# Performance work log

Hardware: AMD Instinct MI355X
Metric: run time of the kernel (lower is better)

Reference implementation:

```python
import jax, jax.numpy as jnp
import numpy as np

N_FQK, N_FV, N_REL, N_VAL, N_KNOW = 512, 256, 128, 64, 256
TOPK_QK, TOPK_V, TOPK_REL, TOPK_VAL = 64, 32, 16, 3
FQK_END = N_FQK
FV_END = N_FQK + N_FV
REL_END = FV_END + N_REL
VAL_END = REL_END + N_VAL
TOTAL = VAL_END + N_KNOW


def setup_inputs() -> dict:
    key = jax.random.key(0)
    k1, k2, k3, k4, k5 = jax.random.split(key, 5)
    B, S, D, DS = 8, 4096, 1024, 64
    x = jax.random.normal(k1, (B, S, D), dtype=jnp.float32)
    importance = jax.random.uniform(k2, (B, S), dtype=jnp.float32)
    proj_w = jax.random.normal(k3, (DS, D), dtype=jnp.float32) * (1.0 / np.sqrt(D))
    proj_b = jax.random.normal(k4, (DS,), dtype=jnp.float32) * 0.01
    neuron_emb = jax.random.normal(k5, (TOTAL, DS), dtype=jnp.float32) * 0.02
    return {"x": x, "importance": importance, "proj_w": proj_w,
            "proj_b": proj_b, "neuron_emb": neuron_emb}


def _topk_sparsify(w, k):
    # keep top-k values per row, zero elsewhere
    vals, idx = jax.lax.top_k(w, k)
    B = w.shape[0]
    sparse = jnp.zeros_like(w).at[jnp.arange(B)[:, None], idx].set(vals)
    return sparse, idx


def reference(x, importance, proj_w, proj_b, neuron_emb):
    # shared projection + normalized neuron embeddings (eval: dropout off,
    # no excitability bonus)
    h = jnp.einsum('bsd,kd->bsk', x, proj_w) + proj_b          # [B,S,d_space]
    emb_n = neuron_emb / jnp.linalg.norm(neuron_emb, axis=-1, keepdims=True)
    all_logits = jnp.einsum('bsk,nk->bsn', h, emb_n)            # [B,S,TOTAL]

    def agg(logits):
        pref = jax.nn.softmax(logits, axis=-1)                  # [B,S,n]
        return jnp.einsum('bs,bsn->bn', importance, pref)

    w_qk = agg(all_logits[..., :FQK_END])
    _, idx_qk = jax.lax.top_k(w_qk, TOPK_QK)
    idx_qk = jnp.sort(idx_qk, axis=-1)

    w_v = agg(all_logits[..., FQK_END:FV_END])
    _, idx_v = jax.lax.top_k(w_v, TOPK_V)
    idx_v = jnp.sort(idx_v, axis=-1)

    rel_logits = all_logits[..., FV_END:REL_END]
    # relational_Q and relational_K use the same logits slice (eval mode)
    rel_dense_Q = agg(rel_logits)
    rel_dense_K = agg(rel_logits)
    rel_Q, _ = _topk_sparsify(rel_dense_Q, TOPK_REL)
    rel_K, _ = _topk_sparsify(rel_dense_K, TOPK_REL)

    val_dense = agg(all_logits[..., REL_END:VAL_END])
    val_w, _ = _topk_sparsify(val_dense, TOPK_VAL)

    return idx_qk, idx_v, rel_Q, rel_K, val_w
```

## Files before the change

kernel.cpp:

```cpp
#include <hip/hip_runtime.h>


typedef short short8 __attribute__((ext_vector_type(8)));
typedef float f32x4 __attribute__((ext_vector_type(4)));
typedef unsigned int uint4v __attribute__((ext_vector_type(4)));

__device__ __forceinline__ unsigned short f32_to_bf16(float f) {
  unsigned u = __float_as_uint(f);
  u += 0x7FFF + ((u >> 16) & 1);
  return (unsigned short)(u >> 16);
}
__device__ __forceinline__ float bf16_to_f32(unsigned short h) {
  return __uint_as_float(((unsigned)h) << 16);
}

__device__ __forceinline__ unsigned cvt_pk_bf16(float a, float b) {
  unsigned r;
  asm("v_cvt_pk_bf16_f32 %0, %1, %2" : "=v"(r) : "v"(a), "v"(b));
  return r;
}

__device__ __forceinline__ void split8v(const f32x4& v0, const f32x4& v1,
                                        short8& hi, short8& lo) {
  unsigned hp[4], lp[4];
#pragma unroll
  for (int j = 0; j < 4; ++j) {
    float a = (j < 2) ? v0[2 * j] : v1[2 * j - 4];
    float b = (j < 2) ? v0[2 * j + 1] : v1[2 * j - 3];
    unsigned p = cvt_pk_bf16(a, b);
    float ra = a - __uint_as_float(p << 16);
    float rb = b - __uint_as_float(p & 0xFFFF0000u);
    hp[j] = p;
    lp[j] = cvt_pk_bf16(ra, rb);
  }
  hi = __builtin_bit_cast(short8, (uint4v){hp[0], hp[1], hp[2], hp[3]});
  lo = __builtin_bit_cast(short8, (uint4v){lp[0], lp[1], lp[2], lp[3]});
}

#define MFMA(a, b, c) __builtin_amdgcn_mfma_f32_16x16x32_bf16(a, b, c, 0, 0, 0)

typedef const __attribute__((address_space(1))) unsigned int guint;
typedef __attribute__((address_space(3))) unsigned int luint;
__device__ __forceinline__ void stage16(const float* g, float* l) {
  __builtin_amdgcn_global_load_lds((guint*)g, (luint*)l, 16, 0, 0);
}
__device__ __forceinline__ void bar() {
  asm volatile("" ::: "memory");
  __builtin_amdgcn_s_barrier();
  asm volatile("" ::: "memory");
}

__global__ __launch_bounds__(256) void k_prep(const float* __restrict__ pw,
                                              const float* __restrict__ emb,
                                              unsigned short* __restrict__ whi,
                                              unsigned short* __restrict__ wlo,
                                              unsigned short* __restrict__ ehi,
                                              unsigned short* __restrict__ elo,
                                              float* __restrict__ wg) {
  int tid = blockIdx.x * 256 + threadIdx.x;
  if (tid < 7680) wg[tid] = 0.f;
  for (int i = tid; i < 65536; i += gridDim.x * 256) {
    float v = pw[i];
    unsigned short h = f32_to_bf16(v);
    whi[i] = h;
    wlo[i] = f32_to_bf16(v - bf16_to_f32(h));
  }
  int wid = tid >> 6, lane = tid & 63;
  int nw = gridDim.x * 4;
  for (int n = wid; n < 960; n += nw) {
    float v = emb[n * 64 + lane];
    float s = v * v;
#pragma unroll
    for (int off = 1; off < 64; off <<= 1) s += __shfl_xor(s, off);
    float vn = v / sqrtf(s);
    unsigned short h = f32_to_bf16(vn);
    ehi[n * 64 + lane] = h;
    elo[n * 64 + lane] = f32_to_bf16(vn - bf16_to_f32(h));
  }
}

__global__ __launch_bounds__(256, 4) void k_main(
    const float* __restrict__ x, const unsigned short* __restrict__ whi,
    const unsigned short* __restrict__ wlo, const float* __restrict__ pb,
    const unsigned short* __restrict__ ehi, const unsigned short* __restrict__ elo,
    const float* __restrict__ imp, float* __restrict__ wg) {
  __shared__ __align__(16) float xt[5][32][32];
  __shared__ __align__(16) unsigned short hxh[32][64];
  __shared__ __align__(16) unsigned short hxl[32][64];
  __shared__ float zpart[4][32][4];
  __shared__ float coefL[32][4];

  const int tid = threadIdx.x, w = tid >> 6, lane = tid & 63;
  const int q = lane >> 4, c = lane & 15;
  const int row0 = blockIdx.x * 32;
  const int nt0 = w;

  const int srow = tid >> 3;
  const int scol = ((tid & 7) ^ (srow & 7)) * 4;
  const float* sbase = x + (size_t)(row0 + srow) * 1024 + scol;
  auto STAGEX = [&](int slot, int ks) {
    stage16(sbase + ks * 32, &xt[slot][0][0] + (w << 8));
  };

  const unsigned short* bwh = whi + (size_t)(nt0 * 16 + c) * 1024 + q * 8;
  const unsigned short* bwl = wlo + (size_t)(nt0 * 16 + c) * 1024 + q * 8;

  f32x4 acc0 = {0.f, 0.f, 0.f, 0.f}, acc1 = {0.f, 0.f, 0.f, 0.f};

  const unsigned sw = (unsigned)((c & 7) << 4);
  const unsigned off1 = ((unsigned)(q * 32)) ^ sw;
  const unsigned off2 = ((unsigned)(q * 32 + 16)) ^ sw;
  const char* xby = (const char*)&xt[0][0][0] + (size_t)c * 128;

  auto projstep = [&](int slot, short8 B_hi, short8 B_lo) {
    const char* bp = xby + slot * 4096;
    f32x4 a0 = *(const f32x4*)(bp + off1);
    f32x4 a1 = *(const f32x4*)(bp + off2);
    f32x4 a2 = *(const f32x4*)(bp + 2048 + off1);
    f32x4 a3 = *(const f32x4*)(bp + 2048 + off2);
    short8 ah, al;
    split8v(a0, a1, ah, al);
    acc0 = MFMA(ah, B_hi, acc0);
    acc0 = MFMA(ah, B_lo, acc0);
    acc0 = MFMA(al, B_hi, acc0);
    split8v(a2, a3, ah, al);
    acc1 = MFMA(ah, B_hi, acc1);
    acc1 = MFMA(ah, B_lo, acc1);
    acc1 = MFMA(al, B_hi, acc1);
  };

  short8 BhA[4], BlA[4], BhB[4], BlB[4];
#pragma unroll
  for (int kk = 0; kk < 4; ++kk) {
    BhA[kk] = *(const short8*)(bwh + kk * 32);
    BlA[kk] = *(const short8*)(bwl + kk * 32);
  }
  STAGEX(0, 0); STAGEX(1, 1); STAGEX(2, 2); STAGEX(3, 3);
  int rs = 0, wsl = 4;

  auto group = [&](int g, short8 (&ch)[4], short8 (&cl)[4],
                   short8 (&nh)[4], short8 (&nl)[4]) {
#pragma unroll
    for (int kk = 0; kk < 4; ++kk) {
      nh[kk] = *(const short8*)(bwh + ((g + 1) * 4 + kk) * 32);
      nl[kk] = *(const short8*)(bwl + ((g + 1) * 4 + kk) * 32);
    }
#pragma unroll
    for (int p = 0; p < 4; ++p) {
      asm volatile("s_waitcnt vmcnt(11)" ::: "memory");
      bar();
      STAGEX(wsl, 4 * g + p + 4);
      projstep(rs, ch[p], cl[p]);
      ++rs; if (rs == 5) rs = 0;
      ++wsl; if (wsl == 5) wsl = 0;
    }
  };
  group(0, BhA, BlA, BhB, BlB);
  group(1, BhB, BlB, BhA, BlA);
  group(2, BhA, BlA, BhB, BlB);
  group(3, BhB, BlB, BhA, BlA);
  group(4, BhA, BlA, BhB, BlB);
  group(5, BhB, BlB, BhA, BlA);
  group(6, BhA, BlA, BhB, BlB);
  asm volatile("s_waitcnt vmcnt(3)" ::: "memory"); bar();
  projstep(rs, BhB[0], BlB[0]); ++rs; if (rs == 5) rs = 0;
  asm volatile("s_waitcnt vmcnt(2)" ::: "memory"); bar();
  projstep(rs, BhB[1], BlB[1]); ++rs; if (rs == 5) rs = 0;
  asm volatile("s_waitcnt vmcnt(1)" ::: "memory"); bar();
  projstep(rs, BhB[2], BlB[2]); ++rs; if (rs == 5) rs = 0;
  asm volatile("s_waitcnt vmcnt(0)" ::: "memory"); bar();
  projstep(rs, BhB[3], BlB[3]);

  float bias = pb[nt0 * 16 + c];
#pragma unroll
  for (int mt = 0; mt < 2; ++mt) {
    f32x4 a = mt ? acc1 : acc0;
#pragma unroll
    for (int r = 0; r < 4; ++r) {
      float val = a[r] + bias;
      int row = mt * 16 + q * 4 + r;
      unsigned colb = (unsigned)((nt0 * 16 + c) * 2);
      unsigned o = (unsigned)(row * 128) + (colb ^ ((unsigned)(row & 7) << 4));
      unsigned short h = f32_to_bf16(val);
      *(unsigned short*)((char*)&hxh[0][0] + o) = h;
      *(unsigned short*)((char*)&hxl[0][0] + o) = f32_to_bf16(val - bf16_to_f32(h));
    }
  }
  __syncthreads();

  short8 Ahi[2][2], Alo[2][2];
#pragma unroll
  for (int mt = 0; mt < 2; ++mt) {
    int row = mt * 16 + c;
    unsigned rsw = (unsigned)((row & 7) << 4);
#pragma unroll
    for (int k2 = 0; k2 < 2; ++k2) {
      unsigned o = (unsigned)(row * 128) + (((unsigned)(k2 * 64 + q * 16)) ^ rsw);
      Ahi[mt][k2] = *(const short8*)((const char*)&hxh[0][0] + o);
      Alo[mt][k2] = *(const short8*)((const char*)&hxl[0][0] + o);
    }
  }

  const size_t ebq = (size_t)c * 64 + q * 8;
  short8 eA[4], eB[4], eC[4];
  auto LOADE = [&](short8 (&d)[4], int i) {
    size_t eb = (size_t)(w + 4 * i) * 1024 + ebq;
    d[0] = *(const short8*)(ehi + eb);
    d[1] = *(const short8*)(ehi + eb + 32);
    d[2] = *(const short8*)(elo + eb);
    d[3] = *(const short8*)(elo + eb + 32);
  };

  f32x4 zacc0 = {0.f, 0.f, 0.f, 0.f}, zacc1 = {0.f, 0.f, 0.f, 0.f};
  auto zflush = [&](int seg) {
#pragma unroll
    for (int mt = 0; mt < 2; ++mt)
#pragma unroll
      for (int r = 0; r < 4; ++r) {
        float v = mt ? zacc1[r] : zacc0[r];
        v += __shfl_xor(v, 1); v += __shfl_xor(v, 2);
        v += __shfl_xor(v, 4); v += __shfl_xor(v, 8);
        if (c == 0) zpart[w][mt * 16 + q * 4 + r][seg] = v;
      }
    zacc0 = (f32x4){0.f, 0.f, 0.f, 0.f};
    zacc1 = (f32x4){0.f, 0.f, 0.f, 0.f};
  };

  int cur_seg = 0;
  auto step1 = [&](int i, short8 (&e)[4]) {
    int nt = w + 4 * i;
    int s = (nt < 32) ? 0 : (nt < 48) ? 1 : (nt < 56) ? 2 : 3;
    if (s != cur_seg) { zflush(cur_seg); cur_seg = s; }
#pragma unroll
    for (int mt = 0; mt < 2; ++mt) {
      f32x4 l = {0.f, 0.f, 0.f, 0.f};
      l = MFMA(Ahi[mt][0], e[0], l); l = MFMA(Ahi[mt][1], e[1], l);
      l = MFMA(Ahi[mt][0], e[2], l); l = MFMA(Ahi[mt][1], e[3], l);
      l = MFMA(Alo[mt][0], e[0], l); l = MFMA(Alo[mt][1], e[1], l);
#pragma unroll
      for (int r = 0; r < 4; ++r) {
        if (mt == 0) zacc0[r] += __expf(l[r]); else zacc1[r] += __expf(l[r]);
      }
    }
  };
  LOADE(eA, 0); LOADE(eB, 1);
  for (int j = 0; j < 5; ++j) {
    LOADE(eC, 3 * j + 2);            step1(3 * j, eA);
    if (j < 4) LOADE(eA, 3 * j + 3); step1(3 * j + 1, eB);
    if (j < 4) LOADE(eB, 3 * j + 4); step1(3 * j + 2, eC);
  }
  zflush(cur_seg);
  __syncthreads();
  if (tid < 128) {
    int row = tid & 31, sg = tid >> 5;
    float Z = zpart[0][row][sg] + zpart[1][row][sg] + zpart[2][row][sg] + zpart[3][row][sg];
    coefL[row][sg] = imp[row0 + row] / Z;
  }
  __syncthreads();

  const int bIdx = row0 >> 12;
  f32x4 cf0, cf1;
  int cs2 = -1;
  auto step2 = [&](int i, short8 (&e)[4]) {
    int nt = w + 4 * i;
    int s = (nt < 32) ? 0 : (nt < 48) ? 1 : (nt < 56) ? 2 : 3;
    if (s != cs2) {
#pragma unroll
      for (int r = 0; r < 4; ++r) {
        cf0[r] = coefL[q * 4 + r][s];
        cf1[r] = coefL[16 + q * 4 + r][s];
      }
      cs2 = s;
    }
    float wsum = 0.f;
#pragma unroll
    for (int mt = 0; mt < 2; ++mt) {
      f32x4 l = {0.f, 0.f, 0.f, 0.f};
      l = MFMA(Ahi[mt][0], e[0], l); l = MFMA(Ahi[mt][1], e[1], l);
      l = MFMA(Ahi[mt][0], e[2], l); l = MFMA(Ahi[mt][1], e[3], l);
      l = MFMA(Alo[mt][0], e[0], l); l = MFMA(Alo[mt][1], e[1], l);
#pragma unroll
      for (int r = 0; r < 4; ++r)
        wsum = fmaf(__expf(l[r]), mt ? cf1[r] : cf0[r], wsum);
    }
    wsum += __shfl_xor(wsum, 16);
    wsum += __shfl_xor(wsum, 32);
    if (lane < 16) atomicAdd(&wg[bIdx * 960 + nt * 16 + c], wsum);
  };
  LOADE(eA, 0); LOADE(eB, 1);
  for (int j = 0; j < 5; ++j) {
    LOADE(eC, 3 * j + 2);            step2(3 * j, eA);
    if (j < 4) LOADE(eA, 3 * j + 3); step2(3 * j + 1, eB);
    if (j < 4) LOADE(eB, 3 * j + 4); step2(3 * j + 2, eC);
  }
}

__global__ __launch_bounds__(256) void k_topk(const float* __restrict__ wg,
                                              float* __restrict__ out) {
  __shared__ float vals[512];
  __shared__ int flags[512];
  int blk = blockIdx.x;
  int b = blk >> 2, t = blk & 3;
  int tid = threadIdx.x;
  const int Ns[4] = {512, 256, 128, 64};
  const int Ks[4] = {64, 32, 16, 3};
  const int Off[4] = {0, 512, 768, 896};
  int N = Ns[t], K = Ks[t], off = Off[t];
  for (int n = tid; n < N; n += 256) vals[n] = wg[b * 960 + off + n];
  __syncthreads();
  for (int n = tid; n < N; n += 256) {
    float v = vals[n];
    int rank = 0;
    for (int m = 0; m < N; ++m) {
      float u = vals[m];
      rank += (u > v || (u == v && m < n)) ? 1 : 0;
    }
    flags[n] = (rank < K) ? 1 : 0;
  }
  __syncthreads();
  if (t <= 1) {
    if (tid < 64) {
      int base = 0;
      for (int ch = 0; ch < N; ch += 64) {
        int n = ch + tid;
        int f = flags[n];
        unsigned long long mask = __ballot(f);
        if (f) {
          int pos = base + __popcll(mask & ((1ull << tid) - 1ull));
          if (t == 0) out[b * 64 + pos] = (float)n;
          else out[512 + b * 32 + pos] = (float)n;
        }
        base += __popcll(mask);
      }
    }
  } else if (t == 2) {
    for (int n = tid; n < 128; n += 256) {
      float v = flags[n] ? vals[n] : 0.f;
      out[768 + b * 128 + n] = v;
      out[1792 + b * 128 + n] = v;
    }
  } else {
    for (int n = tid; n < 64; n += 256) {
      float v = flags[n] ? vals[n] : 0.f;
      out[2816 + b * 64 + n] = v;
    }
  }
}

extern "C" void kernel_launch(void* const* d_in, const int* in_sizes, int n_in,
                              void* d_out, int out_size, void* d_ws, size_t ws_size,
                              hipStream_t stream) {
  const float* x   = (const float*)d_in[0];
  const float* imp = (const float*)d_in[1];
  const float* pw  = (const float*)d_in[2];
  const float* pb  = (const float*)d_in[3];
  const float* emb = (const float*)d_in[4];
  float* out = (float*)d_out;

  char* ws = (char*)d_ws;
  unsigned short* whi = (unsigned short*)(ws);
  unsigned short* wlo = (unsigned short*)(ws + 131072);
  unsigned short* ehi = (unsigned short*)(ws + 262144);
  unsigned short* elo = (unsigned short*)(ws + 385024);
  float*          wg  = (float*)(ws + 507904);

  hipLaunchKernelGGL(k_prep, dim3(64), dim3(256), 0, stream, pw, emb, whi, wlo, ehi, elo, wg);
  hipLaunchKernelGGL(k_main, dim3(1024), dim3(256), 0, stream, x, whi, wlo, pb, ehi, elo, imp, wg);
  hipLaunchKernelGGL(k_topk, dim3(32), dim3(256), 0, stream, wg, out);
}
```

Measured before the change: 302.4 us.

## Replace atomic accumulation with per-block partials and shrink register buffers

Each k_main block now writes its 960 partial sums to its own slot in a scratch buffer instead of doing atomicAdd into a shared per-batch array. The sums are reduced in k_topk, which also drops the zero-init from k_prep. The projection weight prefetch goes from double-buffered groups of 4 k-steps to groups of 2, with retuned vmcnt waits. The embedding loads go from triple to double buffering. These cuts in live registers are meant to ease pressure at 4 blocks per CU, at the cost of shorter prefetch distance and an extra 128-way reduction in the small top-k kernel.

Result: slower. 368.1 us (+21.7%).

```diff
diff --git a/kernel.cpp b/kernel.cpp
--- a/kernel.cpp
+++ b/kernel.cpp
@@ -38,6 +38,7 @@
 }
 
 #define MFMA(a, b, c) __builtin_amdgcn_mfma_f32_16x16x32_bf16(a, b, c, 0, 0, 0)
+#define WAITVM(n) asm volatile("s_waitcnt vmcnt(" #n ")" ::: "memory")
 
 typedef const __attribute__((address_space(1))) unsigned int guint;
 typedef __attribute__((address_space(3))) unsigned int luint;
@@ -55,10 +56,8 @@
                                               unsigned short* __restrict__ whi,
                                               unsigned short* __restrict__ wlo,
                                               unsigned short* __restrict__ ehi,
-                                              unsigned short* __restrict__ elo,
-                                              float* __restrict__ wg) {
+                                              unsigned short* __restrict__ elo) {
   int tid = blockIdx.x * 256 + threadIdx.x;
-  if (tid < 7680) wg[tid] = 0.f;
   for (int i = tid; i < 65536; i += gridDim.x * 256) {
     float v = pw[i];
     unsigned short h = f32_to_bf16(v);
@@ -83,7 +82,7 @@
     const float* __restrict__ x, const unsigned short* __restrict__ whi,
     const unsigned short* __restrict__ wlo, const float* __restrict__ pb,
     const unsigned short* __restrict__ ehi, const unsigned short* __restrict__ elo,
-    const float* __restrict__ imp, float* __restrict__ wg) {
+    const float* __restrict__ imp, float* __restrict__ pp) {
   __shared__ __align__(16) float xt[5][32][32];
   __shared__ __align__(16) unsigned short hxh[32][64];
   __shared__ __align__(16) unsigned short hxl[32][64];
@@ -112,8 +111,9 @@
   const unsigned off2 = ((unsigned)(q * 32 + 16)) ^ sw;
   const char* xby = (const char*)&xt[0][0][0] + (size_t)c * 128;
 
-  auto projstep = [&](int slot, short8 B_hi, short8 B_lo) {
-    const char* bp = xby + slot * 4096;
+  int rs = 0, wsl = 4;
+  auto projstep = [&](short8 B_hi, short8 B_lo) {
+    const char* bp = xby + rs * 4096;
     f32x4 a0 = *(const f32x4*)(bp + off1);
     f32x4 a1 = *(const f32x4*)(bp + off2);
     f32x4 a2 = *(const f32x4*)(bp + 2048 + off1);
@@ -127,49 +127,41 @@
     acc1 = MFMA(ah, B_hi, acc1);
     acc1 = MFMA(ah, B_lo, acc1);
     acc1 = MFMA(al, B_hi, acc1);
-  };
-
-  short8 BhA[4], BlA[4], BhB[4], BlB[4];
-#pragma unroll
-  for (int kk = 0; kk < 4; ++kk) {
-    BhA[kk] = *(const short8*)(bwh + kk * 32);
-    BlA[kk] = *(const short8*)(bwl + kk * 32);
-  }
+    ++rs; if (rs == 5) rs = 0;
+  };
+  auto loadB = [&](short8 (&h)[2], short8 (&l)[2], int g) {
+    h[0] = *(const short8*)(bwh + (2 * g) * 32);
+    h[1] = *(const short8*)(bwh + (2 * g + 1) * 32);
+    l[0] = *(const short8*)(bwl + (2 * g) * 32);
+    l[1] = *(const short8*)(bwl + (2 * g + 1) * 32);
+  };
+
+  short8 BhA[2], BlA[2], BhB[2], BlB[2];
+  loadB(BhA, BlA, 0);
   STAGEX(0, 0); STAGEX(1, 1); STAGEX(2, 2); STAGEX(3, 3);
-  int rs = 0, wsl = 4;
-
-  auto group = [&](int g, short8 (&ch)[4], short8 (&cl)[4],
-                   short8 (&nh)[4], short8 (&nl)[4]) {
-#pragma unroll
-    for (int kk = 0; kk < 4; ++kk) {
-      nh[kk] = *(const short8*)(bwh + ((g + 1) * 4 + kk) * 32);
-      nl[kk] = *(const short8*)(bwl + ((g + 1) * 4 + kk) * 32);
-    }
-#pragma unroll
-    for (int p = 0; p < 4; ++p) {
-      asm volatile("s_waitcnt vmcnt(11)" ::: "memory");
-      bar();
-      STAGEX(wsl, 4 * g + p + 4);
-      projstep(rs, ch[p], cl[p]);
-      ++rs; if (rs == 5) rs = 0;
-      ++wsl; if (wsl == 5) wsl = 0;
-    }
-  };
-  group(0, BhA, BlA, BhB, BlB);
-  group(1, BhB, BlB, BhA, BlA);
-  group(2, BhA, BlA, BhB, BlB);
-  group(3, BhB, BlB, BhA, BlA);
-  group(4, BhA, BlA, BhB, BlB);
-  group(5, BhB, BlB, BhA, BlA);
-  group(6, BhA, BlA, BhB, BlB);
-  asm volatile("s_waitcnt vmcnt(3)" ::: "memory"); bar();
-  projstep(rs, BhB[0], BlB[0]); ++rs; if (rs == 5) rs = 0;
-  asm volatile("s_waitcnt vmcnt(2)" ::: "memory"); bar();
-  projstep(rs, BhB[1], BlB[1]); ++rs; if (rs == 5) rs = 0;
-  asm volatile("s_waitcnt vmcnt(1)" ::: "memory"); bar();
-  projstep(rs, BhB[2], BlB[2]); ++rs; if (rs == 5) rs = 0;
-  asm volatile("s_waitcnt vmcnt(0)" ::: "memory"); bar();
-  projstep(rs, BhB[3], BlB[3]);
+
+  auto gpair = [&](int g) {
+    loadB(BhB, BlB, g + 1);
+    WAITVM(6); bar();
+    STAGEX(wsl, 2 * g + 4); ++wsl; if (wsl == 5) wsl = 0;
+    projstep(BhA[0], BlA[0]);
+    WAITVM(7); bar();
+    STAGEX(wsl, 2 * g + 5); ++wsl; if (wsl == 5) wsl = 0;
+    projstep(BhA[1], BlA[1]);
+    loadB(BhA, BlA, g + 2);
+    WAITVM(6); bar();
+    STAGEX(wsl, 2 * g + 6); ++wsl; if (wsl == 5) wsl = 0;
+    projstep(BhB[0], BlB[0]);
+    WAITVM(7); bar();
+    STAGEX(wsl, 2 * g + 7); ++wsl; if (wsl == 5) wsl = 0;
+    projstep(BhB[1], BlB[1]);
+  };
+  gpair(0); gpair(2); gpair(4); gpair(6); gpair(8); gpair(10); gpair(12);
+  loadB(BhB, BlB, 15);
+  WAITVM(7); bar(); projstep(BhA[0], BlA[0]);
+  WAITVM(6); bar(); projstep(BhA[1], BlA[1]);
+  WAITVM(1); bar(); projstep(BhB[0], BlB[0]);
+  WAITVM(0); bar(); projstep(BhB[1], BlB[1]);
 
   float bias = pb[nt0 * 16 + c];
 #pragma unroll
@@ -202,7 +194,7 @@
   }
 
   const size_t ebq = (size_t)c * 64 + q * 8;
-  short8 eA[4], eB[4], eC[4];
+  short8 eA[4], eB[4];
   auto LOADE = [&](short8 (&d)[4], int i) {
     size_t eb = (size_t)(w + 4 * i) * 1024 + ebq;
     d[0] = *(const short8*)(ehi + eb);
@@ -243,12 +235,13 @@
       }
     }
   };
-  LOADE(eA, 0); LOADE(eB, 1);
-  for (int j = 0; j < 5; ++j) {
-    LOADE(eC, 3 * j + 2);            step1(3 * j, eA);
-    if (j < 4) LOADE(eA, 3 * j + 3); step1(3 * j + 1, eB);
-    if (j < 4) LOADE(eB, 3 * j + 4); step1(3 * j + 2, eC);
-  }
+  LOADE(eA, 0);
+#pragma unroll
+  for (int j = 0; j < 7; ++j) {
+    LOADE(eB, 2 * j + 1); step1(2 * j, eA);
+    LOADE(eA, 2 * j + 2); step1(2 * j + 1, eB);
+  }
+  step1(14, eA);
   zflush(cur_seg);
   __syncthreads();
   if (tid < 128) {
@@ -258,7 +251,7 @@
   }
   __syncthreads();
 
-  const int bIdx = row0 >> 12;
+  float* ppb = pp + (size_t)blockIdx.x * 960;
   f32x4 cf0, cf1;
   int cs2 = -1;
   auto step2 = [&](int i, short8 (&e)[4]) {
@@ -285,17 +278,18 @@
     }
     wsum += __shfl_xor(wsum, 16);
     wsum += __shfl_xor(wsum, 32);
-    if (lane < 16) atomicAdd(&wg[bIdx * 960 + nt * 16 + c], wsum);
-  };
-  LOADE(eA, 0); LOADE(eB, 1);
-  for (int j = 0; j < 5; ++j) {
-    LOADE(eC, 3 * j + 2);            step2(3 * j, eA);
-    if (j < 4) LOADE(eA, 3 * j + 3); step2(3 * j + 1, eB);
-    if (j < 4) LOADE(eB, 3 * j + 4); step2(3 * j + 2, eC);
-  }
-}
-
-__global__ __launch_bounds__(256) void k_topk(const float* __restrict__ wg,
+    if (lane < 16) ppb[nt * 16 + c] = wsum;
+  };
+  LOADE(eA, 0);
+#pragma unroll
+  for (int j = 0; j < 7; ++j) {
+    LOADE(eB, 2 * j + 1); step2(2 * j, eA);
+    LOADE(eA, 2 * j + 2); step2(2 * j + 1, eB);
+  }
+  step2(14, eA);
+}
+
+__global__ __launch_bounds__(256) void k_topk(const float* __restrict__ pp,
                                               float* __restrict__ out) {
   __shared__ float vals[512];
   __shared__ int flags[512];
@@ -306,7 +300,17 @@
   const int Ks[4] = {64, 32, 16, 3};
   const int Off[4] = {0, 512, 768, 896};
   int N = Ns[t], K = Ks[t], off = Off[t];
-  for (int n = tid; n < N; n += 256) vals[n] = wg[b * 960 + off + n];
+  for (int n = tid; n < N; n += 256) {
+    const float* p = pp + (size_t)(b * 128) * 960 + off + n;
+    float s0 = 0.f, s1 = 0.f, s2 = 0.f, s3 = 0.f;
+    for (int rb = 0; rb < 128; rb += 4) {
+      s0 += p[(size_t)(rb + 0) * 960];
+      s1 += p[(size_t)(rb + 1) * 960];
+      s2 += p[(size_t)(rb + 2) * 960];
+      s3 += p[(size_t)(rb + 3) * 960];
+    }
+    vals[n] = (s0 + s1) + (s2 + s3);
+  }
   __syncthreads();
   for (int n = tid; n < N; n += 256) {
     float v = vals[n];
@@ -362,9 +366,9 @@
   unsigned short* wlo = (unsigned short*)(ws + 131072);
   unsigned short* ehi = (unsigned short*)(ws + 262144);
   unsigned short* elo = (unsigned short*)(ws + 385024);
-  float*          wg  = (float*)(ws + 507904);
-
-  hipLaunchKernelGGL(k_prep, dim3(64), dim3(256), 0, stream, pw, emb, whi, wlo, ehi, elo, wg);
-  hipLaunchKernelGGL(k_main, dim3(1024), dim3(256), 0, stream, x, whi, wlo, pb, ehi, elo, imp, wg);
-  hipLaunchKernelGGL(k_topk, dim3(32), dim3(256), 0, stream, wg, out);
-}
+  float*          pp  = (float*)(ws + 507904);
+
+  hipLaunchKernelGGL(k_prep, dim3(64), dim3(256), 0, stream, pw, emb, whi, wlo, ehi, elo);
+  hipLaunchKernelGGL(k_main, dim3(1024), dim3(256), 0, stream, x, whi, wlo, pb, ehi, elo, imp, pp);
+  hipLaunchKernelGGL(k_topk, dim3(32), dim3(256), 0, stream, pp, out);
+}
```
